# Kernel tuning notes

Measured on AMD Instinct MI355X. Metric: run time of the kernel, lower is better.

The kernel has to match this reference:

```python
import jax, jax.numpy as jnp
import numpy as np

B, THETA_DIM, Y_DIM, OUT_DIM, WIDTH, NUM_BLOCKS, MULT = 16384, 64, 16, 256, 1024, 4, 2
EPS = 1e-5


def setup_inputs() -> dict:
    key = jax.random.key(0)
    ks = jax.random.split(key, 16)
    hid = MULT * WIDTH
    in_dim = THETA_DIM + 1 + Y_DIM
    inp = {
        "theta_n": jax.random.normal(ks[0], (B, THETA_DIM), jnp.float32),
        "lambda_n": jax.random.normal(ks[1], (B, 1), jnp.float32),
        "y_oh": jax.random.uniform(ks[2], (B, Y_DIM), jnp.float32),
        # input layer
        "W_in": jax.random.normal(ks[3], (in_dim, WIDTH), jnp.float32) * 0.02,
        "b_in": jnp.zeros((WIDTH,), jnp.float32),
        # stacked ResBlockLN params [num_blocks, ...]
        "ln_g": jnp.ones((NUM_BLOCKS, WIDTH), jnp.float32),
        "ln_b": jnp.zeros((NUM_BLOCKS, WIDTH), jnp.float32),
        "w1": jax.random.normal(ks[4], (NUM_BLOCKS, WIDTH, hid), jnp.float32) * 0.02,
        "b1": jnp.zeros((NUM_BLOCKS, hid), jnp.float32),
        "w2": jax.random.normal(ks[5], (NUM_BLOCKS, hid, WIDTH), jnp.float32) * 0.02,
        "b2": jnp.zeros((NUM_BLOCKS, WIDTH), jnp.float32),
        "res_scale": jnp.full((NUM_BLOCKS,), 0.1, jnp.float32),
        # per-class heads stacked [y_dim, width, out_dim]
        "Wh": jax.random.normal(ks[6], (Y_DIM, WIDTH, OUT_DIM), jnp.float32) * 0.02,
        "bh": jnp.zeros((Y_DIM, OUT_DIM), jnp.float32),
    }
    return inp


def _layernorm(x, g, b):
    mu = jnp.mean(x, axis=-1, keepdims=True)
    var = jnp.mean(jnp.square(x - mu), axis=-1, keepdims=True)
    return (x - mu) * jax.lax.rsqrt(var + EPS) * g + b


def reference(theta_n, lambda_n, y_oh, W_in, b_in, ln_g, ln_b, w1, b1, w2, b2, res_scale, Wh, bh):
    x = jnp.concatenate([theta_n, lambda_n, y_oh], axis=1)  # [B, theta+1+y]
    h = jax.nn.gelu(x @ W_in + b_in, approximate=False)      # [B, width]
    for i in range(NUM_BLOCKS):
        z = _layernorm(h, ln_g[i], ln_b[i])
        z = jax.nn.silu(z @ w1[i] + b1[i])
        z = z @ w2[i] + b2[i]
        h = h + res_scale[i] * z
    y_int = jnp.argmax(y_oh, axis=1)                         # [B]
    # compute all heads, then per-sample gather (argmax-routed head)
    all_out = jnp.einsum("bd,kdo->bko", h, Wh) + bh          # [B, y_dim, out_dim]
    out = jnp.take_along_axis(all_out, y_int[:, None, None], axis=1)[:, 0, :]
    return out
```

## Files before the change

kernel.cpp:

```cpp
#include <hip/hip_runtime.h>
#include <hip/hip_bf16.h>
#include <cstdint>
#include <cstddef>

#define B_ROWS 16384
#define WIDTH  1024
#define HID    2048
#define NBLK   4
#define YDIM   16
#define OUTD   256
#define KIN    128
#define MAXM_PER_CLASS 4096

typedef __attribute__((ext_vector_type(8))) short short8;
typedef __attribute__((ext_vector_type(4))) float f32x4;

__device__ __forceinline__ unsigned short f2bf(float f) {
    union { float f; uint32_t u; } v; v.f = f;
    uint32_t u = v.u;
    uint32_t r = (u + 0x7FFFu + ((u >> 16) & 1u)) >> 16;
    return (unsigned short)r;
}

__device__ __forceinline__ void gload_lds16(const void* g, void* l) {
    __builtin_amdgcn_global_load_lds(
        (const __attribute__((address_space(1))) void*)g,
        (__attribute__((address_space(3))) void*)l, 16, 0, 0);
}

__global__ __launch_bounds__(256)
void prep_x_k(const float* __restrict__ theta, const float* __restrict__ lam,
              const float* __restrict__ yoh, unsigned short* __restrict__ xb)
{
    int tid = threadIdx.x;
    int row = blockIdx.x * 2 + (tid >> 7);
    int j = tid & 127;
    float v;
    if (j < 64)       v = theta[(size_t)row * 64 + j];
    else if (j == 64) v = lam[row];
    else if (j < 81)  v = yoh[(size_t)row * 16 + (j - 65)];
    else              v = 0.f;
    xb[(size_t)row * KIN + j] = f2bf(v);
}

__global__ __launch_bounds__(256)
void bucket_k(const float* __restrict__ yoh, int* __restrict__ counts,
              int* __restrict__ bucket)
{
    __shared__ int cnt_lds[16];
    __shared__ int base_lds[16];
    int tid = threadIdx.x;
    if (tid < 16) cnt_lds[tid] = 0;
    __syncthreads();
    int row = blockIdx.x * 256 + tid;
    const float4* yr = (const float4*)(yoh + (size_t)row * 16);
    int best = 0; float bv = -3.0e38f;
    #pragma unroll
    for (int p = 0; p < 4; ++p) {
        float4 v = yr[p];
        if (v.x > bv) { bv = v.x; best = p * 4 + 0; }
        if (v.y > bv) { bv = v.y; best = p * 4 + 1; }
        if (v.z > bv) { bv = v.z; best = p * 4 + 2; }
        if (v.w > bv) { bv = v.w; best = p * 4 + 3; }
    }
    int mypos = atomicAdd(&cnt_lds[best], 1);
    __syncthreads();
    if (tid < 16) base_lds[tid] = atomicAdd(&counts[tid * 32], cnt_lds[tid]);
    __syncthreads();
    int pos = base_lds[best] + mypos;
    if (pos < MAXM_PER_CLASS) bucket[best * MAXM_PER_CLASS + pos] = row;
}

__global__ __launch_bounds__(256)
void tcvt_k(const float* __restrict__ src, unsigned short* __restrict__ dst,
            int R, int C, int RP)
{
    int b = blockIdx.z;
    src += (size_t)b * R * C;
    dst += (size_t)b * C * RP;
    __shared__ float tile[32][33];
    int tx = threadIdx.x & 31, ty = threadIdx.x >> 5;
    int c0 = blockIdx.x * 32, r0 = blockIdx.y * 32;
    #pragma unroll
    for (int p = 0; p < 4; ++p) {
        int r = r0 + p * 8 + ty;
        float v = (r < R) ? src[(size_t)r * C + c0 + tx] : 0.f;
        tile[p * 8 + ty][tx] = v;
    }
    __syncthreads();
    #pragma unroll
    for (int p = 0; p < 4; ++p) {
        int c = c0 + p * 8 + ty;
        dst[(size_t)c * RP + r0 + tx] = f2bf(tile[tx][p * 8 + ty]);
    }
}

__global__ __launch_bounds__(256)
void ln_k(const float* __restrict__ h, const float* __restrict__ g,
          const float* __restrict__ bb, unsigned short* __restrict__ z)
{
    int row = blockIdx.x;
    int t = threadIdx.x;
    const float4 v = ((const float4*)(h + (size_t)row * WIDTH))[t];
    float s  = v.x + v.y + v.z + v.w;
    float s2 = v.x * v.x + v.y * v.y + v.z * v.z + v.w * v.w;
    #pragma unroll
    for (int off = 32; off > 0; off >>= 1) {
        s  += __shfl_down(s, off);
        s2 += __shfl_down(s2, off);
    }
    __shared__ float red[8];
    int wv = t >> 6;
    if ((t & 63) == 0) { red[wv] = s; red[4 + wv] = s2; }
    __syncthreads();
    float st = 0.f, s2t = 0.f;
    #pragma unroll
    for (int i = 0; i < 4; ++i) { st += red[i]; s2t += red[4 + i]; }
    float mu  = st * (1.f / 1024.f);
    float var = s2t * (1.f / 1024.f) - mu * mu;
    float rs  = rsqrtf(var + 1e-5f);
    float4 gg  = ((const float4*)g)[t];
    float4 bbv = ((const float4*)bb)[t];
    ushort4 o;
    o.x = f2bf((v.x - mu) * rs * gg.x + bbv.x);
    o.y = f2bf((v.y - mu) * rs * gg.y + bbv.y);
    o.z = f2bf((v.z - mu) * rs * gg.z + bbv.z);
    o.w = f2bf((v.w - mu) * rs * gg.w + bbv.w);
    ((ushort4*)(z + (size_t)row * WIDTH))[t] = o;
}

template<int EPI>
__global__ __launch_bounds__(256)
void gemm_k(const short* __restrict__ A, const short* __restrict__ BT,
            const float* __restrict__ bias,
            float* __restrict__ Cf, unsigned short* __restrict__ Cb,
            const float* __restrict__ rs_ptr, int rs_idx, int writeHb,
            const int* __restrict__ counts, const int* __restrict__ bucket,
            float* __restrict__ outp,
            int N, int K, int ntN)
{
    __shared__ short lsA[2][128 * 64];
    __shared__ short lsB[2][128 * 64];
    __shared__ int rowsLds[128];

    int tid = threadIdx.x;
    int w = tid >> 6, lane = tid & 63;

    int bm = 0, bn = 0, m0 = 0, cnt = 0;
    if (EPI == 3) {
        int cls = blockIdx.z;
        cnt = counts[cls * 32];
        if (cnt > MAXM_PER_CLASS) cnt = MAXM_PER_CLASS;
        m0 = blockIdx.y * 128;
        if (m0 >= cnt) return;
        bn = blockIdx.x;
        if (tid < 128) rowsLds[tid] = bucket[cls * MAXM_PER_CLASS + m0 + tid];
        __syncthreads();
        BT   += (size_t)cls * OUTD * WIDTH;
        bias += cls * OUTD;
    } else {
        int nwg = gridDim.x;
        int wg  = blockIdx.x;
        int cpx = nwg >> 3;
        int swz = (wg & 7) * cpx + (wg >> 3);
        bm = swz / ntN; bn = swz % ntN;
    }

    const int sr = lane >> 3;
    const int ss = lane & 7;
    const int wm = w >> 1, wn = w & 1;
    const int nkt = K >> 6;

    f32x4 acc[4][4];
    #pragma unroll
    for (int i = 0; i < 4; ++i)
        #pragma unroll
        for (int j = 0; j < 4; ++j) acc[i][j] = (f32x4)(0.f);

    auto STAGE = [&](int buf, int kt) {
        #pragma unroll
        for (int c = 0; c < 4; ++c) {
            int r  = w * 32 + c * 8 + sr;
            int sg = ss ^ (r & 7);
            long grow = (EPI == 3) ? (long)rowsLds[r] : ((long)bm * 128 + r);
            const short* ga = A + (size_t)grow * K + (size_t)kt * 64 + sg * 8;
            gload_lds16(ga, &lsA[buf][(w * 32 + c * 8) * 64]);
        }
        #pragma unroll
        for (int c = 0; c < 4; ++c) {
            int r  = w * 32 + c * 8 + sr;
            int sg = ss ^ (r & 7);
            const short* gb = BT + (size_t)(bn * 128 + r) * K + (size_t)kt * 64 + sg * 8;
            gload_lds16(gb, &lsB[buf][(w * 32 + c * 8) * 64]);
        }
    };

    STAGE(0, 0);
    asm volatile("s_waitcnt vmcnt(0)" ::: "memory");
    __builtin_amdgcn_s_barrier();

    int cur = 0;
    for (int kt = 0; kt < nkt; ++kt) {
        if (kt + 1 < nkt) STAGE(cur ^ 1, kt + 1);

        #pragma unroll
        for (int ks = 0; ks < 2; ++ks) {
            short8 af[4], bf[4];
            #pragma unroll
            for (int m = 0; m < 4; ++m) {
                int r = wm * 64 + m * 16 + (lane & 15);
                int s = ks * 4 + (lane >> 4);
                af[m] = *(const short8*)&lsA[cur][r * 64 + (s ^ (r & 7)) * 8];
            }
            #pragma unroll
            for (int n = 0; n < 4; ++n) {
                int r = wn * 64 + n * 16 + (lane & 15);
                int s = ks * 4 + (lane >> 4);
                bf[n] = *(const short8*)&lsB[cur][r * 64 + (s ^ (r & 7)) * 8];
            }
            __builtin_amdgcn_s_setprio(1);
            #pragma unroll
            for (int m = 0; m < 4; ++m)
                #pragma unroll
                for (int n = 0; n < 4; ++n)
                    acc[m][n] = __builtin_amdgcn_mfma_f32_16x16x32_bf16(af[m], bf[n], acc[m][n], 0, 0, 0);
            __builtin_amdgcn_s_setprio(0);
        }

        asm volatile("s_waitcnt vmcnt(0)" ::: "memory");
        __builtin_amdgcn_s_barrier();
        cur ^= 1;
    }

    float rscale = (EPI == 2) ? rs_ptr[rs_idx] : 0.f;
    #pragma unroll
    for (int m = 0; m < 4; ++m) {
        #pragma unroll
        for (int reg = 0; reg < 4; ++reg) {
            int lr = wm * 64 + m * 16 + (lane >> 4) * 4 + reg;
            #pragma unroll
            for (int n = 0; n < 4; ++n) {
                int lc = wn * 64 + n * 16 + (lane & 15);
                float v = acc[m][n][reg];
                if (EPI == 0) {
                    size_t idx = ((size_t)bm * 128 + lr) * (size_t)N + bn * 128 + lc;
                    float x = v + bias[bn * 128 + lc];
                    Cf[idx] = 0.5f * x * (1.f + erff(x * 0.70710678118f));
                } else if (EPI == 1) {
                    size_t idx = ((size_t)bm * 128 + lr) * (size_t)N + bn * 128 + lc;
                    float x = v + bias[bn * 128 + lc];
                    Cb[idx] = f2bf(x / (1.f + __expf(-x)));
                } else if (EPI == 2) {
                    size_t idx = ((size_t)bm * 128 + lr) * (size_t)N + bn * 128 + lc;
                    float x = v + bias[bn * 128 + lc];
                    float hv = Cf[idx] + rscale * x;
                    Cf[idx] = hv;
                    if (writeHb) Cb[idx] = f2bf(hv);
                } else {
                    if (m0 + lr < cnt) {
                        int orow = rowsLds[lr];
                        int oc = bn * 128 + lc;
                        outp[(size_t)orow * OUTD + oc] = v + bias[oc];
                    }
                }
            }
        }
    }
}

extern "C" void kernel_launch(void* const* d_in, const int* in_sizes, int n_in,
                              void* d_out, int out_size, void* d_ws, size_t ws_size,
                              hipStream_t stream)
{
    const float* theta = (const float*)d_in[0];
    const float* lam   = (const float*)d_in[1];
    const float* yoh   = (const float*)d_in[2];
    const float* W_in  = (const float*)d_in[3];
    const float* b_in  = (const float*)d_in[4];
    const float* ln_g  = (const float*)d_in[5];
    const float* ln_b  = (const float*)d_in[6];
    const float* w1    = (const float*)d_in[7];
    const float* b1    = (const float*)d_in[8];
    const float* w2    = (const float*)d_in[9];
    const float* b2    = (const float*)d_in[10];
    const float* rsc   = (const float*)d_in[11];
    const float* Wh    = (const float*)d_in[12];
    const float* bh    = (const float*)d_in[13];
    float* out = (float*)d_out;

    char* p = (char*)d_ws;
    auto alloc = [&](size_t bytes) -> char* {
        char* r = p; p += (bytes + 255) & ~(size_t)255; return r;
    };
    float*          h    = (float*)         alloc((size_t)B_ROWS * WIDTH * 4);
    unsigned short* hb   = (unsigned short*)alloc((size_t)B_ROWS * WIDTH * 2);
    unsigned short* z    = (unsigned short*)alloc((size_t)B_ROWS * WIDTH * 2);
    unsigned short* t    = (unsigned short*)alloc((size_t)B_ROWS * HID * 2);
    unsigned short* xb   = (unsigned short*)alloc((size_t)B_ROWS * KIN * 2);
    unsigned short* w1T  = (unsigned short*)alloc((size_t)NBLK * HID * WIDTH * 2);
    unsigned short* w2T  = (unsigned short*)alloc((size_t)NBLK * WIDTH * HID * 2);
    unsigned short* WhT  = (unsigned short*)alloc((size_t)YDIM * OUTD * WIDTH * 2);
    unsigned short* WiT  = (unsigned short*)alloc((size_t)WIDTH * KIN * 2);
    int*            bucket = (int*)alloc((size_t)YDIM * MAXM_PER_CLASS * 4);
    int*            counts = (int*)alloc(16 * 32 * 4);

    hipMemsetAsync(bucket, 0, (size_t)YDIM * MAXM_PER_CLASS * 4, stream);
    hipMemsetAsync(counts, 0, 16 * 32 * 4, stream);

    prep_x_k<<<B_ROWS / 2, 256, 0, stream>>>(theta, lam, yoh, xb);
    bucket_k<<<B_ROWS / 256, 256, 0, stream>>>(yoh, counts, bucket);

    tcvt_k<<<dim3(WIDTH / 32, KIN / 32, 1),    256, 0, stream>>>(W_in, WiT, 81,   WIDTH, KIN);
    tcvt_k<<<dim3(HID / 32,   WIDTH / 32, 4),  256, 0, stream>>>(w1,   w1T, WIDTH, HID,  WIDTH);
    tcvt_k<<<dim3(WIDTH / 32, HID / 32, 4),    256, 0, stream>>>(w2,   w2T, HID,  WIDTH, HID);
    tcvt_k<<<dim3(OUTD / 32,  WIDTH / 32, 16), 256, 0, stream>>>(Wh,   WhT, WIDTH, OUTD, WIDTH);

    gemm_k<0><<<(B_ROWS / 128) * (WIDTH / 128), 256, 0, stream>>>(
        (const short*)xb, (const short*)WiT, b_in, h, nullptr,
        nullptr, 0, 0, nullptr, nullptr, nullptr, WIDTH, KIN, WIDTH / 128);

    for (int i = 0; i < NBLK; ++i) {
        ln_k<<<B_ROWS, 256, 0, stream>>>(h, ln_g + i * WIDTH, ln_b + i * WIDTH, z);
        gemm_k<1><<<(B_ROWS / 128) * (HID / 128), 256, 0, stream>>>(
            (const short*)z, (const short*)(w1T + (size_t)i * HID * WIDTH), b1 + i * HID,
            nullptr, t, nullptr, 0, 0, nullptr, nullptr, nullptr, HID, WIDTH, HID / 128);
        gemm_k<2><<<(B_ROWS / 128) * (WIDTH / 128), 256, 0, stream>>>(
            (const short*)t, (const short*)(w2T + (size_t)i * WIDTH * HID), b2 + i * WIDTH,
            h, hb, rsc, i, (i == NBLK - 1) ? 1 : 0, nullptr, nullptr, nullptr,
            WIDTH, HID, WIDTH / 128);
    }

    gemm_k<3><<<dim3(OUTD / 128, MAXM_PER_CLASS / 128, YDIM), 256, 0, stream>>>(
        (const short*)hb, (const short*)WhT, bh, nullptr, nullptr,
        nullptr, 0, 0, counts, bucket, out, OUTD, WIDTH, OUTD / 128);

    (void)in_sizes; (void)n_in; (void)out_size; (void)ws_size; (void)rsc;
}
```

Baseline: 1.058 ms.

## Add 256x256-tile 512-thread GEMM for residual-block matmuls

Adds a new GEMM kernel with 256x256 output tiles, 8 waves, and a 128x64 per-wave sub-tile. It is used for both the SiLU up-projection and the residual down-projection in every block. The larger tile raises arithmetic intensity and cuts global and LDS traffic per MFMA, and a workgroup index swizzle groups tiles across XCDs. In exchange the kernel needs about 128KB of double-buffered LDS and 128 accumulator registers per thread, which limits occupancy to about one workgroup per CU. The down-projection grid drops to 256 workgroups, which risks poor load balance.

```diff
diff --git a/kernel.cpp b/kernel.cpp
--- a/kernel.cpp
+++ b/kernel.cpp
@@ -130,11 +130,118 @@
 }
 
 template<int EPI>
+__global__ __launch_bounds__(512, 2)
+void gemm256_k(const short* __restrict__ A, const short* __restrict__ BT,
+               const float* __restrict__ bias,
+               float* __restrict__ Cf, unsigned short* __restrict__ Cb,
+               const float* __restrict__ rs_ptr, int rs_idx, int writeHb,
+               int N, int K, int ntN)
+{
+    __shared__ short lsA[2][256 * 64];
+    __shared__ short lsB[2][256 * 64];
+
+    int tid = threadIdx.x;
+    int w = tid >> 6, lane = tid & 63;
+
+    int nwg = gridDim.x;
+    int wg  = blockIdx.x;
+    int cpx = nwg >> 3;
+    int swz = (wg & 7) * cpx + (wg >> 3);
+    int bm = swz / ntN, bn = swz % ntN;
+
+    const int wm = w >> 2, wn = w & 3;
+    const int lr8 = lane >> 3;
+    const int ls8 = lane & 7;
+    const int nkt = K >> 6;
+
+    f32x4 acc[8][4];
+    #pragma unroll
+    for (int i = 0; i < 8; ++i)
+        #pragma unroll
+        for (int j = 0; j < 4; ++j) acc[i][j] = (f32x4)(0.f);
+
+    auto STAGE = [&](int buf, int kt) {
+        #pragma unroll
+        for (int c = 0; c < 4; ++c) {
+            int r  = c * 64 + w * 8 + lr8;
+            int sg = ls8 ^ (r & 7);
+            const short* ga = A + (size_t)(bm * 256 + r) * K + (size_t)kt * 64 + sg * 8;
+            gload_lds16(ga, &lsA[buf][(c * 64 + w * 8) * 64]);
+        }
+        #pragma unroll
+        for (int c = 0; c < 4; ++c) {
+            int r  = c * 64 + w * 8 + lr8;
+            int sg = ls8 ^ (r & 7);
+            const short* gb = BT + (size_t)(bn * 256 + r) * K + (size_t)kt * 64 + sg * 8;
+            gload_lds16(gb, &lsB[buf][(c * 64 + w * 8) * 64]);
+        }
+    };
+
+    STAGE(0, 0);
+    asm volatile("s_waitcnt vmcnt(0)" ::: "memory");
+    __builtin_amdgcn_s_barrier();
+
+    int cur = 0;
+    for (int kt = 0; kt < nkt; ++kt) {
+        if (kt + 1 < nkt) STAGE(cur ^ 1, kt + 1);
+
+        #pragma unroll
+        for (int ks = 0; ks < 2; ++ks) {
+            short8 af[8], bf[4];
+            int s = ks * 4 + (lane >> 4);
+            #pragma unroll
+            for (int m = 0; m < 8; ++m) {
+                int r = wm * 128 + m * 16 + (lane & 15);
+                af[m] = *(const short8*)&lsA[cur][r * 64 + (s ^ (r & 7)) * 8];
+            }
+            #pragma unroll
+            for (int n = 0; n < 4; ++n) {
+                int r = wn * 64 + n * 16 + (lane & 15);
+                bf[n] = *(const short8*)&lsB[cur][r * 64 + (s ^ (r & 7)) * 8];
+            }
+            __builtin_amdgcn_s_setprio(1);
+            #pragma unroll
+            for (int m = 0; m < 8; ++m)
+                #pragma unroll
+                for (int n = 0; n < 4; ++n)
+                    acc[m][n] = __builtin_amdgcn_mfma_f32_16x16x32_bf16(af[m], bf[n], acc[m][n], 0, 0, 0);
+            __builtin_amdgcn_s_setprio(0);
+        }
+
+        asm volatile("s_waitcnt vmcnt(0)" ::: "memory");
+        __builtin_amdgcn_s_barrier();
+        cur ^= 1;
+    }
+
+    float rscale = (EPI == 2) ? rs_ptr[rs_idx] : 0.f;
+    #pragma unroll
+    for (int m = 0; m < 8; ++m) {
+        #pragma unroll
+        for (int reg = 0; reg < 4; ++reg) {
+            int lr = wm * 128 + m * 16 + (lane >> 4) * 4 + reg;
+            #pragma unroll
+            for (int n = 0; n < 4; ++n) {
+                int lc = wn * 64 + n * 16 + (lane & 15);
+                float v = acc[m][n][reg];
+                size_t idx = ((size_t)bm * 256 + lr) * (size_t)N + bn * 256 + lc;
+                float x = v + bias[bn * 256 + lc];
+                if (EPI == 1) {
+                    Cb[idx] = f2bf(x / (1.f + __expf(-x)));
+                } else {
+                    float hv = Cf[idx] + rscale * x;
+                    Cf[idx] = hv;
+                    if (writeHb) Cb[idx] = f2bf(hv);
+                }
+            }
+        }
+    }
+}
+
+template<int EPI>
 __global__ __launch_bounds__(256)
 void gemm_k(const short* __restrict__ A, const short* __restrict__ BT,
             const float* __restrict__ bias,
-            float* __restrict__ Cf, unsigned short* __restrict__ Cb,
-            const float* __restrict__ rs_ptr, int rs_idx, int writeHb,
+            float* __restrict__ Cf,
             const int* __restrict__ counts, const int* __restrict__ bucket,
             float* __restrict__ outp,
             int N, int K, int ntN)
@@ -232,7 +339,6 @@
         cur ^= 1;
     }
 
-    float rscale = (EPI == 2) ? rs_ptr[rs_idx] : 0.f;
     #pragma unroll
     for (int m = 0; m < 4; ++m) {
         #pragma unroll
@@ -246,16 +352,6 @@
                     size_t idx = ((size_t)bm * 128 + lr) * (size_t)N + bn * 128 + lc;
                     float x = v + bias[bn * 128 + lc];
                     Cf[idx] = 0.5f * x * (1.f + erff(x * 0.70710678118f));
-                } else if (EPI == 1) {
-                    size_t idx = ((size_t)bm * 128 + lr) * (size_t)N + bn * 128 + lc;
-                    float x = v + bias[bn * 128 + lc];
-                    Cb[idx] = f2bf(x / (1.f + __expf(-x)));
-                } else if (EPI == 2) {
-                    size_t idx = ((size_t)bm * 128 + lr) * (size_t)N + bn * 128 + lc;
-                    float x = v + bias[bn * 128 + lc];
-                    float hv = Cf[idx] + rscale * x;
-                    Cf[idx] = hv;
-                    if (writeHb) Cb[idx] = f2bf(hv);
                 } else {
                     if (m0 + lr < cnt) {
                         int orow = rowsLds[lr];
@@ -316,23 +412,22 @@
     tcvt_k<<<dim3(OUTD / 32,  WIDTH / 32, 16), 256, 0, stream>>>(Wh,   WhT, WIDTH, OUTD, WIDTH);
 
     gemm_k<0><<<(B_ROWS / 128) * (WIDTH / 128), 256, 0, stream>>>(
-        (const short*)xb, (const short*)WiT, b_in, h, nullptr,
-        nullptr, 0, 0, nullptr, nullptr, nullptr, WIDTH, KIN, WIDTH / 128);
+        (const short*)xb, (const short*)WiT, b_in, h,
+        nullptr, nullptr, nullptr, WIDTH, KIN, WIDTH / 128);
 
     for (int i = 0; i < NBLK; ++i) {
         ln_k<<<B_ROWS, 256, 0, stream>>>(h, ln_g + i * WIDTH, ln_b + i * WIDTH, z);
-        gemm_k<1><<<(B_ROWS / 128) * (HID / 128), 256, 0, stream>>>(
+        gemm256_k<1><<<(B_ROWS / 256) * (HID / 256), 512, 0, stream>>>(
             (const short*)z, (const short*)(w1T + (size_t)i * HID * WIDTH), b1 + i * HID,
-            nullptr, t, nullptr, 0, 0, nullptr, nullptr, nullptr, HID, WIDTH, HID / 128);
-        gemm_k<2><<<(B_ROWS / 128) * (WIDTH / 128), 256, 0, stream>>>(
+            nullptr, t, nullptr, 0, 0, HID, WIDTH, HID / 256);
+        gemm256_k<2><<<(B_ROWS / 256) * (WIDTH / 256), 512, 0, stream>>>(
             (const short*)t, (const short*)(w2T + (size_t)i * WIDTH * HID), b2 + i * WIDTH,
-            h, hb, rsc, i, (i == NBLK - 1) ? 1 : 0, nullptr, nullptr, nullptr,
-            WIDTH, HID, WIDTH / 128);
+            h, hb, rsc, i, (i == NBLK - 1) ? 1 : 0, WIDTH, HID, WIDTH / 256);
     }
 
     gemm_k<3><<<dim3(OUTD / 128, MAXM_PER_CLASS / 128, YDIM), 256, 0, stream>>>(
-        (const short*)hb, (const short*)WhT, bh, nullptr, nullptr,
-        nullptr, 0, 0, counts, bucket, out, OUTD, WIDTH, OUTD / 128);
+        (const short*)hb, (const short*)WhT, bh, nullptr,
+        counts, bucket, out, OUTD, WIDTH, OUTD / 128);
 
     (void)in_sizes; (void)n_in; (void)out_size; (void)ws_size; (void)rsc;
 }
```

Result: faster. 1.013 ms (-4.3%).
